# Kernel optimization log

Measured on AMD Instinct MI355X. Metric: run time of the kernel, lower is better.

The kernel has to match this reference:

```python
import jax, jax.numpy as jnp
import numpy as np
import math

MARGIN = 0.5
SCALE = 64.0
CURVATURE = 1.0
COS_M = math.cos(MARGIN)
SIN_M = math.sin(MARGIN)
TH = math.cos(math.pi - MARGIN)
MM = math.sin(math.pi - MARGIN) * MARGIN

B, D, C = 2048, 512, 16384


def setup_inputs() -> dict:
    key = jax.random.key(0)
    k1, k2, k3 = jax.random.split(key, 3)
    embeddings = jax.random.normal(k1, (B, D), dtype=jnp.float32) * 0.05  # roughly inside the ball
    labels = jax.random.randint(k2, (B,), 0, C)
    # xavier_uniform for [C, D]
    limit = math.sqrt(6.0 / (C + D))
    weight = jax.random.uniform(k3, (C, D), dtype=jnp.float32, minval=-limit, maxval=limit)
    return {"embeddings": embeddings, "labels": labels, "weight": weight}


def _exp_map_zero(v, c):
    sqrt_c = c ** 0.5
    v_norm = jnp.maximum(jnp.linalg.norm(v, axis=-1, keepdims=True), 1e-7)
    return jnp.tanh(sqrt_c * v_norm) * v / (sqrt_c * v_norm)


def reference(embeddings, labels, weight):
    c = CURVATURE
    # class prototypes mapped onto the Poincare ball, clipped to radius 0.95
    proto = _exp_map_zero(weight, c)                                  # [C, D]
    proto_norm = jnp.linalg.norm(proto, axis=-1, keepdims=True)
    proto = jnp.where(proto_norm > 0.95, proto * 0.95 / proto_norm, proto)

    x = embeddings                                                     # [B, D]
    x_sq = jnp.sum(x * x, axis=-1)                                    # [B]
    y_sq = jnp.sum(proto * proto, axis=-1)                            # [C]
    xy = x @ proto.T                                                  # [B, C]
    diff_sq = jnp.maximum(x_sq[:, None] + y_sq[None, :] - 2.0 * xy, 0.0)

    x_sq_c = jnp.minimum(x_sq, 1.0 - 1e-5)
    y_sq_c = jnp.minimum(y_sq, 1.0 - 1e-5)
    denom = (1.0 - c * x_sq_c)[:, None] * (1.0 - c * y_sq_c)[None, :]
    arg = 1.0 + 2.0 * c * diff_sq / jnp.maximum(denom, 1e-7)
    dists = jnp.arccosh(jnp.maximum(arg, 1.0 + 1e-7)) / (c ** 0.5)    # [B, C]

    sims = jnp.exp(-dists)
    cosine = jnp.clip(2.0 * sims - 1.0, -1.0, 1.0)
    sine = jnp.sqrt(jnp.maximum(1.0 - cosine * cosine, 1e-7))
    phi = cosine * COS_M - sine * SIN_M
    phi = jnp.where(cosine > TH, phi, cosine - MM)

    one_hot = jax.nn.one_hot(labels, cosine.shape[1], dtype=cosine.dtype)
    logits = (one_hot * phi + (1.0 - one_hot) * cosine) * SCALE        # [B, C]

    logp = jax.nn.log_softmax(logits, axis=-1)
    loss = -jnp.mean(jnp.take_along_axis(logp, labels[:, None], axis=1))
    return loss
```

## Files before the change

### kernel.cpp

```cpp
#include <hip/hip_runtime.h>
#include <math.h>

#define Bn 2048
#define Dn 512
#define Cn 16384

typedef float v4f __attribute__((ext_vector_type(4)));

#define WAIT_VM4()  asm volatile("s_waitcnt vmcnt(4)" ::: "memory")
#define WAIT_VM0()  asm volatile("s_waitcnt vmcnt(0)" ::: "memory")
#define RAW_BAR()   asm volatile("s_barrier" ::: "memory")
#define LGKM0_BAR() asm volatile("s_waitcnt lgkmcnt(0)\n\ts_barrier" ::: "memory")

__device__ __forceinline__ void async16(const void* g, void* l) {
  __builtin_amdgcn_global_load_lds(
      (const __attribute__((address_space(1))) char*)g,
      (__attribute__((address_space(3))) char*)l, 16, 0, 0);
}


__device__ __forceinline__ void prep_load(
    int row, int lane, const float* __restrict__ w, const float* __restrict__ x,
    float4& a, float4& b)
{
  const float* src = (row < Cn) ? (w + (size_t)row * Dn) : (x + (size_t)(row - Cn) * Dn);
  const float4* s4 = (const float4*)src;
  a = s4[lane * 2];
  b = s4[lane * 2 + 1];
}

__device__ __forceinline__ void prep_row_vals(
    int row, int lane, float4 a, float4 b,
    char* __restrict__ wq8, char* __restrict__ xq8,
    float* __restrict__ fscale, float* __restrict__ ysqA, float* __restrict__ yrA,
    float* __restrict__ xsA, float* __restrict__ xrA)
{
  bool isW = row < Cn;
  float ss = a.x * a.x + a.y * a.y + a.z * a.z + a.w * a.w
           + b.x * b.x + b.y * b.y + b.z * b.z + b.w * b.w;
  #pragma unroll
  for (int d = 1; d < 64; d <<= 1) ss += __shfl_xor(ss, d);

  int w0 = __builtin_amdgcn_cvt_pk_fp8_f32(a.x * 16.f, a.y * 16.f, 0, false);
  w0     = __builtin_amdgcn_cvt_pk_fp8_f32(a.z * 16.f, a.w * 16.f, w0, true);
  int w1 = __builtin_amdgcn_cvt_pk_fp8_f32(b.x * 16.f, b.y * 16.f, 0, false);
  w1     = __builtin_amdgcn_cvt_pk_fp8_f32(b.z * 16.f, b.w * 16.f, w1, true);
  char* dst = isW ? (wq8 + (size_t)row * Dn) : (xq8 + (size_t)(row - Cn) * Dn);
  ((int2*)dst)[lane] = make_int2(w0, w1);

  if (lane == 0) {
    if (isW) {
      float n = fmaxf(sqrtf(ss), 1e-7f);
      float e2 = __expf(2.f * fminf(n, 10.f));
      float t = (e2 - 1.f) * __builtin_amdgcn_rcpf(e2 + 1.f);
      float tc = fminf(t, 0.95f);
      fscale[row] = tc / n;
      float ys = tc * tc;
      ysqA[row] = ys;
      yrA[row] = 1.f / (1.f - fminf(ys, 1.f - 1e-5f));
    } else {
      int r = row - Cn;
      xsA[r] = ss;
      xrA[r] = 1.f / (1.f - fminf(ss, 1.f - 1e-5f));
    }
  }
}

__device__ __forceinline__ void gemm_job(
    int job, int tid, char* lds,
    const char* __restrict__ xq8, const char* __restrict__ wq8,
    const float* __restrict__ fscale, const float* __restrict__ ysqA,
    const float* __restrict__ yrA, const float* __restrict__ xsA,
    const float* __restrict__ xrA, float* __restrict__ partials)
{
  const int xcd = job & 7;
  const int loc = job >> 3;
  const int mt  = loc & 15;
  const int nt  = (xcd << 4) | (loc >> 4);
  const int mBase = mt * 128;
  const int nBase = nt * 128;
  const int lane = tid & 63;
  const int wv = tid >> 6;
  const int quad = lane >> 4;
  const int l16 = lane & 15;
  const int waveM = wv >> 1;
  const int waveN = wv & 1;

  v4f acc[4][4];
  #pragma unroll
  for (int i = 0; i < 4; ++i)
    #pragma unroll
    for (int j = 0; j < 4; ++j)
      acc[i][j] = (v4f){0.f, 0.f, 0.f, 0.f};

  const int s0 = tid, s1 = tid + 256;
  const int r0 = s0 >> 2, c0 = (s0 & 3) ^ ((r0 >> 1) & 3);
  const int r1 = s1 >> 2, c1 = (s1 & 3) ^ ((r1 >> 1) & 3);
  const char* gA0 = xq8 + (size_t)(mBase + r0) * Dn + c0 * 16;
  const char* gA1 = xq8 + (size_t)(mBase + r1) * Dn + c1 * 16;
  const char* gW0 = wq8 + (size_t)(nBase + r0) * Dn + c0 * 16;
  const char* gW1 = wq8 + (size_t)(nBase + r1) * Dn + c1 * 16;
  const int lo0 = s0 * 16, lo1 = s1 * 16;

  const int kx = (l16 >> 1) & 3;
  int aoff[2], boff[2];
  #pragma unroll
  for (int s = 0; s < 2; ++s) {
    int chunk = (2 * s + (quad >> 1)) ^ kx;
    aoff[s] = (waveM * 64 + l16) * 64 + chunk * 16 + (quad & 1) * 8;
    boff[s] = (waveN * 64 + l16) * 64 + chunk * 16 + (quad & 1) * 8;
  }

  #pragma unroll
  for (int t = 0; t < 2; ++t) {
    char* Ab = lds + t * 16384;
    char* Wb = Ab + 8192;
    async16(gA0 + t * 64, Ab + lo0);
    async16(gA1 + t * 64, Ab + lo1);
    async16(gW0 + t * 64, Wb + lo0);
    async16(gW1 + t * 64, Wb + lo1);
  }

  #pragma unroll
  for (int kt = 0; kt < 8; ++kt) {
    const int cur = kt & 1;
    if (kt < 7) { WAIT_VM4(); } else { WAIT_VM0(); }
    RAW_BAR();
    char* Ab = lds + cur * 16384;
    char* Wb = Ab + 8192;
    long af[4][2], bf[4][2];
    #pragma unroll
    for (int s = 0; s < 2; ++s) {
      #pragma unroll
      for (int i = 0; i < 4; ++i) af[i][s] = *(const long*)(Ab + aoff[s] + i * 1024);
      #pragma unroll
      for (int j = 0; j < 4; ++j) bf[j][s] = *(const long*)(Wb + boff[s] + j * 1024);
    }
    #pragma unroll
    for (int s = 0; s < 2; ++s)
      #pragma unroll
      for (int i = 0; i < 4; ++i)
        #pragma unroll
        for (int j = 0; j < 4; ++j)
          acc[i][j] = __builtin_amdgcn_mfma_f32_16x16x32_fp8_fp8(af[i][s], bf[j][s], acc[i][j], 0, 0, 0);
    LGKM0_BAR();
    if (kt + 2 < 8) {
      async16(gA0 + (kt + 2) * 64, Ab + lo0);
      async16(gA1 + (kt + 2) * 64, Ab + lo1);
      async16(gW0 + (kt + 2) * 64, Wb + lo0);
      async16(gW1 + (kt + 2) * 64, Wb + lo1);
    }
  }

  float ysqj[4], yrj[4], gj[4];
  #pragma unroll
  for (int j = 0; j < 4; ++j) {
    int col = nBase + waveN * 64 + j * 16 + l16;
    gj[j] = -2.f * fscale[col] * (1.f / 256.f);
    ysqj[j] = ysqA[col];
    yrj[j] = yrA[col];
  }
  #pragma unroll
  for (int i = 0; i < 4; ++i) {
    #pragma unroll
    for (int r = 0; r < 4; ++r) {
      int row = mBase + waveM * 64 + i * 16 + quad * 4 + r;
      float xs = xsA[row];
      float xr2 = 2.f * xrA[row];
      float partial = 0.f;
      if (xs >= 0.99999f) {
        #pragma unroll
        for (int j = 0; j < 4; ++j) {
          float d = fmaxf(fmaf(gj[j], acc[i][j][r], xs + ysqj[j]), 0.f);
          float z = fmaf(d, xr2 * yrj[j], 1.f);
          float u = 64.f * __builtin_amdgcn_rcpf(z);
          partial += fmaf(u, fmaf(0.5f, u, 1.f), 1.f);
        }
      } else {
        #pragma unroll
        for (int j = 0; j < 4; ++j) {
          float d = fmaxf(fmaf(gj[j], acc[i][j][r], xs + ysqj[j]), 0.f);
          float z = fmaf(d, xr2 * yrj[j], 1.f);
          float sq = sqrtf(fmaf(z, z, -1.f));
          float u = 128.f * __builtin_amdgcn_rcpf(z + sq);
          partial += __expf(u);
        }
      }
      partial += __shfl_xor(partial, 1);
      partial += __shfl_xor(partial, 2);
      partial += __shfl_xor(partial, 4);
      partial += __shfl_xor(partial, 8);
      if (l16 == 0) partials[(size_t)row * 256 + nt * 2 + waveN] = partial;
    }
  }
}

__device__ __forceinline__ float final_row_term(
    int row, int lane,
    const float* __restrict__ x, const float* __restrict__ w,
    const int* __restrict__ labels, const float* __restrict__ fscale,
    const float* __restrict__ ysqA, const float* __restrict__ yrA,
    const float* __restrict__ xsA, const float* __restrict__ xrA,
    const float* __restrict__ partials)
{
  const float* pr = partials + (size_t)row * 256;
  float sum = pr[lane] + pr[lane + 64] + pr[lane + 128] + pr[lane + 192];

  int lab = labels[row];
  const float4* xv = (const float4*)(x + (size_t)row * Dn);
  const float4* wv4 = (const float4*)(w + (size_t)lab * Dn);
  float4 a0 = xv[lane * 2], a1 = xv[lane * 2 + 1];
  float4 b0 = wv4[lane * 2], b1 = wv4[lane * 2 + 1];
  float dot = a0.x * b0.x + a0.y * b0.y + a0.z * b0.z + a0.w * b0.w
            + a1.x * b1.x + a1.y * b1.y + a1.z * b1.z + a1.w * b1.w;
  #pragma unroll
  for (int d = 1; d < 64; d <<= 1) {
    sum += __shfl_xor(sum, d);
    dot += __shfl_xor(dot, d);
  }

  float term = 0.f;
  if (lane == 0) {
    float xy = fscale[lab] * dot;
    float diff = fmaxf(xsA[row] + ysqA[lab] - 2.f * xy, 0.f);
    float z = fmaf(2.f * diff, xrA[row] * yrA[lab], 1.f);
    float sq = sqrtf(fmaf(z, z, -1.f));
    float sims = 1.f / (z + sq);
    float u_lab = 128.f * sims;
    float cosv = fmaf(2.f, sims, -1.f);
    float sine = sqrtf(fmaxf(fmaf(-cosv, cosv, 1.f), 1e-7f));
    float phi = (cosv > -0.8775825619f)
                    ? (cosv * 0.8775825619f - sine * 0.4794255386f)
                    : (cosv - 0.2397127693f);
    float e_lab = __expf(u_lab);
    float e_phi = __expf(fminf(64.f * phi + 64.f, 80.f));
    term = logf(sum - e_lab + e_phi) - 64.f * phi - 64.f;
  }
  return term;
}


__global__ __launch_bounds__(256) void prep_kernel(
    const float* __restrict__ w, const float* __restrict__ x,
    char* __restrict__ wq8, char* __restrict__ xq8,
    float* __restrict__ fscale, float* __restrict__ ysqA, float* __restrict__ yrA,
    float* __restrict__ xsA, float* __restrict__ xrA)
{
  int row = (blockIdx.x * 256 + threadIdx.x) >> 6;
  int lane = threadIdx.x & 63;
  float4 a, b;
  prep_load(row, lane, w, x, a, b);
  prep_row_vals(row, lane, a, b, wq8, xq8, fscale, ysqA, yrA, xsA, xrA);
}

__global__ __launch_bounds__(256, 3) void gemm_kernel(
    const char* __restrict__ xq8, const char* __restrict__ wq8,
    const float* __restrict__ fscale, const float* __restrict__ ysqA,
    const float* __restrict__ yrA, const float* __restrict__ xsA,
    const float* __restrict__ xrA, float* __restrict__ partials)
{
  __shared__ int4 ldsv[2048];
  gemm_job(blockIdx.x, threadIdx.x, (char*)ldsv, xq8, wq8, fscale, ysqA, yrA, xsA, xrA, partials);
}

__global__ __launch_bounds__(256) void final_kernel(
    const float* __restrict__ x, const float* __restrict__ w,
    const int* __restrict__ labels, const float* __restrict__ fscale,
    const float* __restrict__ ysqA, const float* __restrict__ yrA,
    const float* __restrict__ xsA, const float* __restrict__ xrA,
    const float* __restrict__ partials, float* __restrict__ out)
{
  int row = blockIdx.x * 4 + (threadIdx.x >> 6);
  float term = final_row_term(row, threadIdx.x & 63, x, w, labels, fscale,
                              ysqA, yrA, xsA, xrA, partials);
  __shared__ float red[4];
  if ((threadIdx.x & 63) == 0) red[threadIdx.x >> 6] = term;
  __syncthreads();
  if (threadIdx.x == 0)
    atomicAdd(out, (red[0] + red[1] + red[2] + red[3]) * (1.f / (float)Bn));
}

extern "C" void kernel_launch(void* const* d_in, const int* in_sizes, int n_in,
                              void* d_out, int out_size, void* d_ws, size_t ws_size,
                              hipStream_t stream) {
  (void)in_sizes; (void)n_in; (void)out_size; (void)ws_size;
  const float* emb = (const float*)d_in[0];
  const int* labels = (const int*)d_in[1];
  const float* weight = (const float*)d_in[2];
  float* out = (float*)d_out;

  char* p = (char*)d_ws;
  char* wq8 = p; p += (size_t)Cn * Dn;
  char* xq8 = p; p += (size_t)Bn * Dn;
  float* fscale = (float*)p; p += (size_t)Cn * 4;
  float* ysqA  = (float*)p; p += (size_t)Cn * 4;
  float* yrA   = (float*)p; p += (size_t)Cn * 4;
  float* xsA   = (float*)p; p += (size_t)Bn * 4;
  float* xrA   = (float*)p; p += (size_t)Bn * 4;
  float* partials = (float*)p; p += (size_t)Bn * 256 * 4;

  hipMemsetAsync(out, 0, sizeof(float), stream);
  prep_kernel<<<(Cn + Bn) / 4, 256, 0, stream>>>(weight, emb, wq8, xq8, fscale, ysqA, yrA, xsA, xrA);
  gemm_kernel<<<(Bn / 128) * (Cn / 128), 256, 0, stream>>>(
      xq8, wq8, fscale, ysqA, yrA, xsA, xrA, partials);
  final_kernel<<<Bn / 4, 256, 0, stream>>>(emb, weight, labels, fscale, ysqA, yrA, xsA, xrA, partials, out);
}
```

Before: 125.9 us.

## Enlarge GEMM tile to 256x256 with triple-buffered LDS and interleaved prefetch

After: 140.9 us. 12.0% more time.

```diff
diff --git a/kernel.cpp b/kernel.cpp
--- a/kernel.cpp
+++ b/kernel.cpp
@@ -10,7 +10,6 @@
 #define WAIT_VM4()  asm volatile("s_waitcnt vmcnt(4)" ::: "memory")
 #define WAIT_VM0()  asm volatile("s_waitcnt vmcnt(0)" ::: "memory")
 #define RAW_BAR()   asm volatile("s_barrier" ::: "memory")
-#define LGKM0_BAR() asm volatile("s_waitcnt lgkmcnt(0)\n\ts_barrier" ::: "memory")
 
 __device__ __forceinline__ void async16(const void* g, void* l) {
   __builtin_amdgcn_global_load_lds(
@@ -66,7 +65,7 @@
   }
 }
 
-__device__ __forceinline__ void gemm_job(
+__device__ __forceinline__ void gemm256_job(
     int job, int tid, char* lds,
     const char* __restrict__ xq8, const char* __restrict__ wq8,
     const float* __restrict__ fscale, const float* __restrict__ ysqA,
@@ -75,112 +74,138 @@
 {
   const int xcd = job & 7;
   const int loc = job >> 3;
-  const int mt  = loc & 15;
-  const int nt  = (xcd << 4) | (loc >> 4);
-  const int mBase = mt * 128;
-  const int nBase = nt * 128;
+  const int mt  = loc >> 3;
+  const int nt  = (xcd << 3) | (loc & 7);
+  const int mBase = mt * 256;
+  const int nBase = nt * 256;
   const int lane = tid & 63;
   const int wv = tid >> 6;
   const int quad = lane >> 4;
   const int l16 = lane & 15;
-  const int waveM = wv >> 1;
-  const int waveN = wv & 1;
-
-  v4f acc[4][4];
-  #pragma unroll
-  for (int i = 0; i < 4; ++i)
+  const int waveM = wv >> 2;
+  const int waveN = wv & 3;
+
+  v4f acc[8][4];
+  #pragma unroll
+  for (int i = 0; i < 8; ++i)
     #pragma unroll
     for (int j = 0; j < 4; ++j)
       acc[i][j] = (v4f){0.f, 0.f, 0.f, 0.f};
 
-  const int s0 = tid, s1 = tid + 256;
-  const int r0 = s0 >> 2, c0 = (s0 & 3) ^ ((r0 >> 1) & 3);
-  const int r1 = s1 >> 2, c1 = (s1 & 3) ^ ((r1 >> 1) & 3);
-  const char* gA0 = xq8 + (size_t)(mBase + r0) * Dn + c0 * 16;
-  const char* gA1 = xq8 + (size_t)(mBase + r1) * Dn + c1 * 16;
-  const char* gW0 = wq8 + (size_t)(nBase + r0) * Dn + c0 * 16;
-  const char* gW1 = wq8 + (size_t)(nBase + r1) * Dn + c1 * 16;
-  const int lo0 = s0 * 16, lo1 = s1 * 16;
+  const int srow = tid >> 2;
+  const int sc = (tid & 3) ^ ((srow >> 1) & 3);
+  const char* gA = xq8 + (size_t)(mBase + srow) * Dn + sc * 16;
+  const char* gB = wq8 + (size_t)(nBase + srow) * Dn + sc * 16;
+  const int loA0 = tid * 16,          loA1 = tid * 16 + 8192;
+  const int loB0 = tid * 16 + 16384,  loB1 = tid * 16 + 24576;
 
   const int kx = (l16 >> 1) & 3;
   int aoff[2], boff[2];
   #pragma unroll
   for (int s = 0; s < 2; ++s) {
     int chunk = (2 * s + (quad >> 1)) ^ kx;
-    aoff[s] = (waveM * 64 + l16) * 64 + chunk * 16 + (quad & 1) * 8;
-    boff[s] = (waveN * 64 + l16) * 64 + chunk * 16 + (quad & 1) * 8;
+    aoff[s] = (waveM * 128 + l16) * 64 + chunk * 16 + (quad & 1) * 8;
+    boff[s] = 16384 + (waveN * 64 + l16) * 64 + chunk * 16 + (quad & 1) * 8;
   }
 
   #pragma unroll
   for (int t = 0; t < 2; ++t) {
-    char* Ab = lds + t * 16384;
-    char* Wb = Ab + 8192;
-    async16(gA0 + t * 64, Ab + lo0);
-    async16(gA1 + t * 64, Ab + lo1);
-    async16(gW0 + t * 64, Wb + lo0);
-    async16(gW1 + t * 64, Wb + lo1);
+    char* buf = lds + t * 32768;
+    async16(gA + t * 64,                       buf + loA0);
+    async16(gA + (size_t)128 * Dn + t * 64,    buf + loA1);
+    async16(gB + t * 64,                       buf + loB0);
+    async16(gB + (size_t)128 * Dn + t * 64,    buf + loB1);
   }
 
   #pragma unroll
   for (int kt = 0; kt < 8; ++kt) {
-    const int cur = kt & 1;
+    char* buf  = lds + (kt % 3) * 32768;
+    char* nbuf = lds + ((kt + 2) % 3) * 32768;
+    const bool pre = (kt + 2 < 8);
     if (kt < 7) { WAIT_VM4(); } else { WAIT_VM0(); }
     RAW_BAR();
-    char* Ab = lds + cur * 16384;
-    char* Wb = Ab + 8192;
-    long af[4][2], bf[4][2];
-    #pragma unroll
-    for (int s = 0; s < 2; ++s) {
-      #pragma unroll
-      for (int i = 0; i < 4; ++i) af[i][s] = *(const long*)(Ab + aoff[s] + i * 1024);
-      #pragma unroll
-      for (int j = 0; j < 4; ++j) bf[j][s] = *(const long*)(Wb + boff[s] + j * 1024);
+
+    long bf[4][2];
+    #pragma unroll
+    for (int n = 0; n < 4; ++n)
+      #pragma unroll
+      for (int s = 0; s < 2; ++s)
+        bf[n][s] = *(const long*)(buf + boff[s] + n * 1024);
+    long af[2][2];
+    #pragma unroll
+    for (int m2 = 0; m2 < 2; ++m2)
+      #pragma unroll
+      for (int s = 0; s < 2; ++s)
+        af[m2][s] = *(const long*)(buf + aoff[s] + m2 * 1024);
+    if (pre) async16(gA + (kt + 2) * 64, nbuf + loA0);
+    __builtin_amdgcn_s_setprio(1);
+    #pragma unroll
+    for (int s = 0; s < 2; ++s)
+      #pragma unroll
+      for (int m2 = 0; m2 < 2; ++m2)
+        #pragma unroll
+        for (int n = 0; n < 4; ++n)
+          acc[m2][n] = __builtin_amdgcn_mfma_f32_16x16x32_fp8_fp8(
+              af[m2][s], bf[n][s], acc[m2][n], 0, 0, 0);
+    __builtin_amdgcn_s_setprio(0);
+    RAW_BAR();
+
+    #pragma unroll
+    for (int q = 1; q < 4; ++q) {
+      #pragma unroll
+      for (int m2 = 0; m2 < 2; ++m2)
+        #pragma unroll
+        for (int s = 0; s < 2; ++s)
+          af[m2][s] = *(const long*)(buf + aoff[s] + (q * 2 + m2) * 1024);
+      if (pre) {
+        if (q == 1) async16(gA + (size_t)128 * Dn + (kt + 2) * 64, nbuf + loA1);
+        if (q == 2) async16(gB + (kt + 2) * 64,                    nbuf + loB0);
+        if (q == 3) async16(gB + (size_t)128 * Dn + (kt + 2) * 64, nbuf + loB1);
+      }
+      RAW_BAR();
+      __builtin_amdgcn_s_setprio(1);
+      #pragma unroll
+      for (int s = 0; s < 2; ++s)
+        #pragma unroll
+        for (int m2 = 0; m2 < 2; ++m2)
+          #pragma unroll
+          for (int n = 0; n < 4; ++n)
+            acc[q * 2 + m2][n] = __builtin_amdgcn_mfma_f32_16x16x32_fp8_fp8(
+                af[m2][s], bf[n][s], acc[q * 2 + m2][n], 0, 0, 0);
+      __builtin_amdgcn_s_setprio(0);
+      RAW_BAR();
     }
-    #pragma unroll
-    for (int s = 0; s < 2; ++s)
-      #pragma unroll
-      for (int i = 0; i < 4; ++i)
-        #pragma unroll
-        for (int j = 0; j < 4; ++j)
-          acc[i][j] = __builtin_amdgcn_mfma_f32_16x16x32_fp8_fp8(af[i][s], bf[j][s], acc[i][j], 0, 0, 0);
-    LGKM0_BAR();
-    if (kt + 2 < 8) {
-      async16(gA0 + (kt + 2) * 64, Ab + lo0);
-      async16(gA1 + (kt + 2) * 64, Ab + lo1);
-      async16(gW0 + (kt + 2) * 64, Wb + lo0);
-      async16(gW1 + (kt + 2) * 64, Wb + lo1);
-    }
   }
 
   float ysqj[4], yrj[4], gj[4];
   #pragma unroll
-  for (int j = 0; j < 4; ++j) {
-    int col = nBase + waveN * 64 + j * 16 + l16;
-    gj[j] = -2.f * fscale[col] * (1.f / 256.f);
-    ysqj[j] = ysqA[col];
-    yrj[j] = yrA[col];
-  }
-  #pragma unroll
-  for (int i = 0; i < 4; ++i) {
+  for (int n = 0; n < 4; ++n) {
+    int col = nBase + waveN * 64 + n * 16 + l16;
+    gj[n] = -2.f * fscale[col] * (1.f / 256.f);
+    ysqj[n] = ysqA[col];
+    yrj[n] = yrA[col];
+  }
+  #pragma unroll
+  for (int m = 0; m < 8; ++m) {
     #pragma unroll
     for (int r = 0; r < 4; ++r) {
-      int row = mBase + waveM * 64 + i * 16 + quad * 4 + r;
+      int row = mBase + waveM * 128 + m * 16 + quad * 4 + r;
       float xs = xsA[row];
       float xr2 = 2.f * xrA[row];
       float partial = 0.f;
       if (xs >= 0.99999f) {
         #pragma unroll
-        for (int j = 0; j < 4; ++j) {
-          float d = fmaxf(fmaf(gj[j], acc[i][j][r], xs + ysqj[j]), 0.f);
-          float z = fmaf(d, xr2 * yrj[j], 1.f);
+        for (int n = 0; n < 4; ++n) {
+          float d = fmaxf(fmaf(gj[n], acc[m][n][r], xs + ysqj[n]), 0.f);
+          float z = fmaf(d, xr2 * yrj[n], 1.f);
           float u = 64.f * __builtin_amdgcn_rcpf(z);
           partial += fmaf(u, fmaf(0.5f, u, 1.f), 1.f);
         }
       } else {
         #pragma unroll
-        for (int j = 0; j < 4; ++j) {
-          float d = fmaxf(fmaf(gj[j], acc[i][j][r], xs + ysqj[j]), 0.f);
-          float z = fmaf(d, xr2 * yrj[j], 1.f);
+        for (int n = 0; n < 4; ++n) {
+          float d = fmaxf(fmaf(gj[n], acc[m][n][r], xs + ysqj[n]), 0.f);
+          float z = fmaf(d, xr2 * yrj[n], 1.f);
           float sq = sqrtf(fmaf(z, z, -1.f));
           float u = 128.f * __builtin_amdgcn_rcpf(z + sq);
           partial += __expf(u);
@@ -190,7 +215,7 @@
       partial += __shfl_xor(partial, 2);
       partial += __shfl_xor(partial, 4);
       partial += __shfl_xor(partial, 8);
-      if (l16 == 0) partials[(size_t)row * 256 + nt * 2 + waveN] = partial;
+      if (l16 == 0) partials[(size_t)row * 256 + nt * 4 + waveN] = partial;
     }
   }
 }
@@ -253,14 +278,15 @@
   prep_row_vals(row, lane, a, b, wq8, xq8, fscale, ysqA, yrA, xsA, xrA);
 }
 
-__global__ __launch_bounds__(256, 3) void gemm_kernel(
+__global__ __launch_bounds__(512, 2) void gemm_kernel(
     const char* __restrict__ xq8, const char* __restrict__ wq8,
     const float* __restrict__ fscale, const float* __restrict__ ysqA,
     const float* __restrict__ yrA, const float* __restrict__ xsA,
     const float* __restrict__ xrA, float* __restrict__ partials)
 {
-  __shared__ int4 ldsv[2048];
-  gemm_job(blockIdx.x, threadIdx.x, (char*)ldsv, xq8, wq8, fscale, ysqA, yrA, xsA, xrA, partials);
+  extern __shared__ int4 ldsv[];
+  gemm256_job(blockIdx.x, threadIdx.x, (char*)ldsv, xq8, wq8,
+              fscale, ysqA, yrA, xsA, xrA, partials);
 }
 
 __global__ __launch_bounds__(256) void final_kernel(
@@ -301,7 +327,7 @@
 
   hipMemsetAsync(out, 0, sizeof(float), stream);
   prep_kernel<<<(Cn + Bn) / 4, 256, 0, stream>>>(weight, emb, wq8, xq8, fscale, ysqA, yrA, xsA, xrA);
-  gemm_kernel<<<(Bn / 128) * (Cn / 128), 256, 0, stream>>>(
+  gemm_kernel<<<(Bn / 256) * (Cn / 256), 512, 3 * 32768, stream>>>(
       xq8, wq8, fscale, ysqA, yrA, xsA, xrA, partials);
   final_kernel<<<Bn / 4, 256, 0, stream>>>(emb, weight, labels, fscale, ysqA, yrA, xsA, xrA, partials, out);
 }
```
